# Kernel optimization log

Hardware: AMD Instinct MI355X
Metric: run time of the kernel (lower is better)

## Reference

```python
import jax, jax.numpy as jnp
import numpy as np

K = 256
L = 1.0 / K
W = L / 2.5


def setup_inputs() -> dict:
    key = jax.random.key(0)
    x = jax.random.uniform(key, (8, 512, 512), dtype=jnp.float32)
    return {"x": x}


def reference(x) -> jnp.ndarray:
    B, H, Wd = x.shape
    N = H * Wd
    mu_k = (L * (jnp.arange(K, dtype=x.dtype) + 0.5))  # [K]
    xf = x.reshape(B, 1, N)                             # [B,1,N]
    d = xf - mu_k[None, :, None]                        # [B,K,N]
    pj = jax.nn.sigmoid((d + L / 2) / W) - jax.nn.sigmoid((d - L / 2) / W)
    return pj.sum(axis=2) / N                           # [B,K]
```

## Files before the change

kernel.cpp:

```cpp
#include <hip/hip_runtime.h>
#include <hip/hip_bf16.h>


constexpr int KBINS   = 256;
constexpr int FSUB    = 16;
constexpr int LPAD    = 64;
constexpr int TAPS    = 145;
constexpr int LDS_FH  = 4360;
constexpr int NPB     = 512 * 512;
constexpr int BLK_PER_BATCH = 32;
constexpr int CHUNK   = NPB / BLK_PER_BATCH;
constexpr int THREADS = 1024;

__device__ __forceinline__ int skew(int p) { return p + (p >> 5); }

__global__ __launch_bounds__(THREADS)
void hist_kernel(const float* __restrict__ x, float* __restrict__ ws) {
    __shared__ unsigned fh[LDS_FH];
    __shared__ float w[TAPS];
    const int tid = threadIdx.x;

    for (int i = tid; i < LDS_FH; i += THREADS) fh[i] = 0u;

    if (tid < TAPS) {
        float a = 0.15625f * (float)(tid - 64);
        float b = 0.15625f * (float)(tid - 80);
        w[tid] = 1.f / (1.f + __expf(-a)) - 1.f / (1.f + __expf(-b));
    }
    __syncthreads();

    const int b     = blockIdx.x / BLK_PER_BATCH;
    const int chunk = blockIdx.x % BLK_PER_BATCH;
    const float4* xv = (const float4*)(x + (size_t)b * NPB + (size_t)chunk * CHUNK);

    #pragma unroll
    for (int it = 0; it < CHUNK / (4 * THREADS); ++it) {
        float4 v = xv[it * THREADS + tid];
        float vals[4] = {v.x, v.y, v.z, v.w};
        int addr[4];
        #pragma unroll
        for (int c = 0; c < 4; ++c) {
            float s = fmaf(vals[c], (float)(KBINS * FSUB), (float)LPAD + 0.5f);
            s = fminf(fmaxf(s, 0.f), 4224.f);
            addr[c] = skew((int)s);
        }
        #pragma unroll
        for (int c = 0; c < 4; ++c)
            atomicAdd(&fh[addr[c]], 1u);
    }
    __syncthreads();

    {
        const int bin = tid >> 2;
        const int q   = tid & 3;
        const int j0  = q * 37;
        const int j1  = (j0 + 37 < TAPS) ? j0 + 37 : TAPS;
        const int base = bin * FSUB;
        float acc = 0.f;
        #pragma unroll 4
        for (int j = j0; j < j1; ++j)
            acc += w[j] * (float)fh[skew(base + j)];
        acc += __shfl_xor(acc, 1);
        acc += __shfl_xor(acc, 2);
        if (q == 0)
            ws[(size_t)blockIdx.x * KBINS + bin] = acc;
    }
}

__global__ __launch_bounds__(KBINS)
void reduce_kernel(const float* __restrict__ ws, float* __restrict__ out) {
    const int b = blockIdx.x;
    const int k = threadIdx.x;
    const float* p = ws + (size_t)b * BLK_PER_BATCH * KBINS + k;
    float s = 0.f;
    #pragma unroll
    for (int c = 0; c < BLK_PER_BATCH; ++c)
        s += p[(size_t)c * KBINS];
    out[b * KBINS + k] = s * (1.f / (float)NPB);
}

extern "C" void kernel_launch(void* const* d_in, const int* in_sizes, int n_in,
                              void* d_out, int out_size, void* d_ws, size_t ws_size,
                              hipStream_t stream) {
    const float* x = (const float*)d_in[0];
    float* out = (float*)d_out;
    float* ws  = (float*)d_ws;
    const int B = in_sizes[0] / NPB;

    hist_kernel<<<B * BLK_PER_BATCH, THREADS, 0, stream>>>(x, ws);
    reduce_kernel<<<B, KBINS, 0, stream>>>(ws, out);
}
```

Before: 59.86 us.

## Replace LDS atomics with per-wave 16-bit histograms using ballot match aggregation

Each wave now owns a private 16-bit histogram row. Within a wave, lanes that fall in the same fine bin are found by a 13-bit ballot match, and only the leader lane does a non-atomic add of the popcount. The per-wave rows are then summed into a shared 32-bit histogram before the convolution with the sigmoid taps. The input loads are also issued before the LDS clearing to overlap their latency. The aim is to remove LDS atomic contention, at the cost of 13 ballots per element, much larger LDS use, and an extra reduction pass.

```diff
diff --git a/kernel.cpp b/kernel.cpp
--- a/kernel.cpp
+++ b/kernel.cpp
@@ -11,42 +11,69 @@
 constexpr int BLK_PER_BATCH = 32;
 constexpr int CHUNK   = NPB / BLK_PER_BATCH;
 constexpr int THREADS = 1024;
+constexpr int NWAVES  = THREADS / 64;
+constexpr int ROWB    = 4360;
 
 __device__ __forceinline__ int skew(int p) { return p + (p >> 5); }
 
 __global__ __launch_bounds__(THREADS)
-void hist_kernel(const float* __restrict__ x, float* __restrict__ ws) {
-    __shared__ unsigned fh[LDS_FH];
+void hist_kernel(const float* __restrict__ x, float* __restrict__ partials) {
+    __shared__ __align__(16) unsigned short fh16[NWAVES][ROWB];
+    __shared__ unsigned fhs[LDS_FH];
     __shared__ float w[TAPS];
-    const int tid = threadIdx.x;
-
-    for (int i = tid; i < LDS_FH; i += THREADS) fh[i] = 0u;
-
-    if (tid < TAPS) {
-        float a = 0.15625f * (float)(tid - 64);
-        float b = 0.15625f * (float)(tid - 80);
-        w[tid] = 1.f / (1.f + __expf(-a)) - 1.f / (1.f + __expf(-b));
-    }
-    __syncthreads();
+    const int tid  = threadIdx.x;
+    const int lane = tid & 63;
+    unsigned short* fw = &fh16[tid >> 6][0];
 
     const int b     = blockIdx.x / BLK_PER_BATCH;
     const int chunk = blockIdx.x % BLK_PER_BATCH;
     const float4* xv = (const float4*)(x + (size_t)b * NPB + (size_t)chunk * CHUNK);
+    const float4 v0 = xv[tid];
+    const float4 v1 = xv[THREADS + tid];
 
-    #pragma unroll
-    for (int it = 0; it < CHUNK / (4 * THREADS); ++it) {
-        float4 v = xv[it * THREADS + tid];
-        float vals[4] = {v.x, v.y, v.z, v.w};
-        int addr[4];
+    {
+        uint4* z = (uint4*)&fh16[0][0];
+        for (int i = tid; i < (NWAVES * ROWB) / 8; i += THREADS)
+            z[i] = make_uint4(0u, 0u, 0u, 0u);
+    }
+    if (tid < TAPS) {
+        float a = 0.15625f * (float)(tid - 64);
+        float c = 0.15625f * (float)(tid - 80);
+        w[tid] = 1.f / (1.f + __expf(-a)) - 1.f / (1.f + __expf(-c));
+    }
+    __syncthreads();
+
+    {
+        const float vals[8] = {v0.x, v0.y, v0.z, v0.w, v1.x, v1.y, v1.z, v1.w};
         #pragma unroll
-        for (int c = 0; c < 4; ++c) {
+        for (int c = 0; c < 8; ++c) {
             float s = fmaf(vals[c], (float)(KBINS * FSUB), (float)LPAD + 0.5f);
             s = fminf(fmaxf(s, 0.f), 4224.f);
-            addr[c] = skew((int)s);
+            const int p = (int)s;
+            unsigned long long m = ~0ull;
+            #pragma unroll
+            for (int bit = 0; bit < 13; ++bit) {
+                const unsigned long long bl = __ballot((p >> bit) & 1);
+                m &= ((p >> bit) & 1) ? bl : ~bl;
+            }
+            if (lane == __ffsll((long long)m) - 1)
+                fw[p] = (unsigned short)(fw[p] + (unsigned)__popcll(m));
         }
+    }
+    __syncthreads();
+
+    for (int t = tid; t < 1057; t += THREADS) {
+        unsigned sx = 0u, sy = 0u;
         #pragma unroll
-        for (int c = 0; c < 4; ++c)
-            atomicAdd(&fh[addr[c]], 1u);
+        for (int wv = 0; wv < NWAVES; ++wv) {
+            const uint2 v = *(const uint2*)&fh16[wv][4 * t];
+            sx += v.x; sy += v.y;
+        }
+        const int p = 4 * t;
+        fhs[skew(p + 0)] = sx & 0xFFFFu;
+        fhs[skew(p + 1)] = sx >> 16;
+        fhs[skew(p + 2)] = sy & 0xFFFFu;
+        fhs[skew(p + 3)] = sy >> 16;
     }
     __syncthreads();
 
@@ -59,19 +86,19 @@
         float acc = 0.f;
         #pragma unroll 4
         for (int j = j0; j < j1; ++j)
-            acc += w[j] * (float)fh[skew(base + j)];
+            acc += w[j] * (float)fhs[skew(base + j)];
         acc += __shfl_xor(acc, 1);
         acc += __shfl_xor(acc, 2);
         if (q == 0)
-            ws[(size_t)blockIdx.x * KBINS + bin] = acc;
+            partials[(size_t)blockIdx.x * KBINS + bin] = acc;
     }
 }
 
 __global__ __launch_bounds__(KBINS)
-void reduce_kernel(const float* __restrict__ ws, float* __restrict__ out) {
+void reduce_kernel(const float* __restrict__ partials, float* __restrict__ out) {
     const int b = blockIdx.x;
     const int k = threadIdx.x;
-    const float* p = ws + (size_t)b * BLK_PER_BATCH * KBINS + k;
+    const float* p = partials + (size_t)b * BLK_PER_BATCH * KBINS + k;
     float s = 0.f;
     #pragma unroll
     for (int c = 0; c < BLK_PER_BATCH; ++c)
@@ -84,9 +111,9 @@
                               hipStream_t stream) {
     const float* x = (const float*)d_in[0];
     float* out = (float*)d_out;
-    float* ws  = (float*)d_ws;
+    float* partials = (float*)d_ws;
     const int B = in_sizes[0] / NPB;
 
-    hist_kernel<<<B * BLK_PER_BATCH, THREADS, 0, stream>>>(x, ws);
-    reduce_kernel<<<B, KBINS, 0, stream>>>(ws, out);
+    hist_kernel<<<B * BLK_PER_BATCH, THREADS, 0, stream>>>(x, partials);
+    reduce_kernel<<<B, KBINS, 0, stream>>>(partials, out);
 }
```

New measurement: 66.82 us. 1.12x slower.
